# Kernel optimization log

Hardware: AMD Instinct MI355X
Metric: run time of the kernel (lower is better)

## Reference

```python
import jax, jax.numpy as jnp
import numpy as np

N = 50000        # nodes
E = 800000       # edges (avg degree 16)
NFEAT = 16       # 14 feat + 2 pos
NHID = 64
NCLASS = 1
NGRAPHS = 500
NLAYERS = 5
DT, ALPHA, GAMMA = 1.0, 1.0, 1.0


def _lin_init(k, fan_in, fan_out):
    # torch nn.Linear default: U(-1/sqrt(fan_in), 1/sqrt(fan_in))
    lim = 1.0 / np.sqrt(fan_in)
    kw, kb = jax.random.split(k)
    W = jax.random.uniform(kw, (fan_in, fan_out), minval=-lim, maxval=lim, dtype=jnp.float32)
    b = jax.random.uniform(kb, (fan_out,), minval=-lim, maxval=lim, dtype=jnp.float32)
    return W, b


def setup_inputs() -> dict:
    key = jax.random.key(0)
    ks = jax.random.split(key, 8)
    x = jax.random.normal(ks[0], (N, 14), dtype=jnp.float32)
    pos = jax.random.normal(ks[1], (N, 2), dtype=jnp.float32)
    edge_index = jax.random.randint(ks[2], (2, E), 0, N, dtype=jnp.int64)
    batch = jnp.sort(jax.random.randint(ks[3], (N,), 0, NGRAPHS, dtype=jnp.int64))
    enc_W, enc_b = _lin_init(ks[4], NFEAT, NHID)
    conv_W, conv_b = _lin_init(ks[5], NHID, NHID)
    res_W, res_b = _lin_init(ks[6], NHID, NHID)
    dec_W, dec_b = _lin_init(ks[7], NHID, NCLASS)
    return dict(x=x, pos=pos, edge_index=edge_index, batch=batch,
                enc_W=enc_W, enc_b=enc_b, conv_W=conv_W, conv_b=conv_b,
                res_W=res_W, res_b=res_b, dec_W=dec_W, dec_b=dec_b)


def _gcn_conv(h, src, dst, W, b):
    # PyG GCNConv: add self-loops, symmetric normalization, scatter-add to dst.
    loop = jnp.arange(N, dtype=src.dtype)
    src2 = jnp.concatenate([src, loop])
    dst2 = jnp.concatenate([dst, loop])
    deg = jax.ops.segment_sum(jnp.ones_like(dst2, dtype=h.dtype), dst2, num_segments=N)
    dinv = jnp.where(deg > 0, jax.lax.rsqrt(deg), 0.0)
    hW = h @ W                                   # [N, nhid]
    norm = dinv[src2] * dinv[dst2]               # [E+N]
    msg = hW[src2] * norm[:, None]               # [E+N, nhid]
    return jax.ops.segment_sum(msg, dst2, num_segments=N) + b


def reference(x, pos, edge_index, batch, enc_W, enc_b, conv_W, conv_b, res_W, res_b, dec_W, dec_b):
    src, dst = edge_index[0], edge_index[1]
    inp = jnp.concatenate([x, pos], axis=-1)     # [N, nfeat]
    Y = inp @ enc_W + enc_b
    X = Y
    # dropout p=0 -> identity (eval mode)
    for _ in range(NLAYERS):
        agg = _gcn_conv(X, src, dst, conv_W, conv_b) + (X @ res_W + res_b)
        Y = Y + DT * (jax.nn.relu(agg) - ALPHA * Y - GAMMA * X)
        X = X + DT * Y
    Xo = X @ dec_W + dec_b                       # [N, 1]
    pooled = jax.ops.segment_sum(Xo, batch, num_segments=NGRAPHS)  # [G, 1]
    return pooled.squeeze(-1)                    # [G]
```

## Files before the change

### kernel.cpp

```cpp
#include <hip/hip_runtime.h>

#define NN 50000
#define NE 800000
#define NH 64
#define NG 500
#define NPAD 50176
#define NBKT 782
#define CAP 1536
#define ZR NN
#define SH 25088

typedef __attribute__((ext_vector_type(8))) short bf16x8;
typedef __attribute__((ext_vector_type(4))) float f32x4;

__device__ __forceinline__ unsigned short f2bf(float f) {
  unsigned x = __float_as_uint(f);
  unsigned r = ((x >> 16) & 1u) + 0x7fffu;
  return (unsigned short)((x + r) >> 16);
}
__device__ __forceinline__ float bf2f(unsigned short u) {
  return __uint_as_float(((unsigned)u) << 16);
}


__global__ __launch_bounds__(256) void k_prep(const float* __restrict__ Wc, const float* __restrict__ Wr,
                                              unsigned short* __restrict__ Wf,
                                              int* __restrict__ bcur,
                                              unsigned short* __restrict__ hWbf) {
  if (blockIdx.x == 8) {
    int tt = threadIdx.x;
    for (int i = tt; i < 1024; i += 256) bcur[i] = 0;
    if (tt < 32) ((unsigned*)(hWbf + (size_t)ZR * 64))[tt] = 0u;
    return;
  }
  int t = blockIdx.x * 256 + threadIdx.x;
  int fid = t >> 6;
  int lane = t & 63;
  int ntile = fid & 3, s = (fid >> 2) & 1, part = (fid >> 3) & 1, mat = fid >> 4;
  const float* W = mat ? Wr : Wc;
  int col = ntile * 16 + (lane & 15);
  int k0 = s * 32 + (lane >> 4) * 8;
#pragma unroll
  for (int e = 0; e < 8; e++) {
    float w = W[(k0 + e) * 64 + col];
    unsigned short h = f2bf(w);
    Wf[(size_t)fid * 512 + lane * 8 + e] = part ? f2bf(w - bf2f(h)) : h;
  }
}


__global__ __launch_bounds__(256) void k_bin(const int* __restrict__ src, const int* __restrict__ dst,
                                             int* __restrict__ bcur, int* __restrict__ colp) {
  __shared__ int hist[NBKT];
  __shared__ int gbase[NBKT];
  int t = threadIdx.x;
  for (int b = t; b < NBKT; b += 256) hist[b] = 0;
  __syncthreads();
  int e0 = blockIdx.x * 8192;
#pragma unroll
  for (int i = 0; i < 32; i++) {
    int e = e0 + i * 256 + t;
    if (e < NE) atomicAdd(&hist[dst[e] >> 6], 1);
  }
  __syncthreads();
  for (int b = t; b < NBKT; b += 256) {
    int c = hist[b];
    gbase[b] = c ? atomicAdd(&bcur[b], c) : 0;
    hist[b] = 0;
  }
  __syncthreads();
#pragma unroll
  for (int i = 0; i < 32; i++) {
    int e = e0 + i * 256 + t;
    if (e < NE) {
      int s = src[e], d = dst[e];
      int b = d >> 6;
      int r = atomicAdd(&hist[b], 1);
      colp[b * CAP + gbase[b] + r] = (s << 6) | (d & 63);
    }
  }
}


template <int MODE>
__device__ __forceinline__ void gemm_tile(int lane, int n0,
                                          const float* __restrict__ Xin,
                                          const unsigned short* __restrict__ gsum,
                                          const unsigned short* __restrict__ Wf,
                                          const float* __restrict__ cb, const float* __restrict__ rb,
                                          const float* __restrict__ dinv,
                                          unsigned short* __restrict__ hWout, float* __restrict__ agg) {
  int col16 = lane & 15;
  int kb = lane >> 4;
  int nr = n0 + col16;
  int nc = nr < NN ? nr : NN - 1;
  const float* xrow = Xin + (size_t)nc * 64;
  float v0[8], v1[8];
  {
    float4 a = *(const float4*)(xrow + kb * 8);
    float4 b4 = *(const float4*)(xrow + kb * 8 + 4);
    float4 c = *(const float4*)(xrow + 32 + kb * 8);
    float4 d = *(const float4*)(xrow + 32 + kb * 8 + 4);
    v0[0] = a.x; v0[1] = a.y; v0[2] = a.z; v0[3] = a.w;
    v0[4] = b4.x; v0[5] = b4.y; v0[6] = b4.z; v0[7] = b4.w;
    v1[0] = c.x; v1[1] = c.y; v1[2] = c.z; v1[3] = c.w;
    v1[4] = d.x; v1[5] = d.y; v1[6] = d.z; v1[7] = d.w;
  }
  if (MODE) {
    float dvn = dinv[nc];
    const unsigned* grow = (const unsigned*)(gsum + (size_t)nc * 64);
    uint4 g0 = *(const uint4*)(grow + kb * 4);
    uint4 g1 = *(const uint4*)(grow + 16 + kb * 4);
    unsigned ga[4] = {g0.x, g0.y, g0.z, g0.w};
    unsigned gb[4] = {g1.x, g1.y, g1.z, g1.w};
#pragma unroll
    for (int e = 0; e < 4; e++) {
      v0[2 * e]     = fmaxf(v0[2 * e]     + dvn * bf2f((unsigned short)(ga[e] & 0xffff)), 0.f);
      v0[2 * e + 1] = fmaxf(v0[2 * e + 1] + dvn * bf2f((unsigned short)(ga[e] >> 16)), 0.f);
      v1[2 * e]     = fmaxf(v1[2 * e]     + dvn * bf2f((unsigned short)(gb[e] & 0xffff)), 0.f);
      v1[2 * e + 1] = fmaxf(v1[2 * e + 1] + dvn * bf2f((unsigned short)(gb[e] >> 16)), 0.f);
    }
  }
  bf16x8 ah0, al0, ah1, al1;
#pragma unroll
  for (int e = 0; e < 8; e++) {
    unsigned short h0 = f2bf(v0[e]);
    ah0[e] = (short)h0;
    al0[e] = (short)f2bf(v0[e] - bf2f(h0));
    unsigned short h1 = f2bf(v1[e]);
    ah1[e] = (short)h1;
    al1[e] = (short)f2bf(v1[e] - bf2f(h1));
  }

  f32x4 aC[4], aR[4];
#pragma unroll
  for (int j = 0; j < 4; j++) {
    aC[j] = (f32x4){0.f, 0.f, 0.f, 0.f};
    aR[j] = (f32x4){0.f, 0.f, 0.f, 0.f};
  }
  const bf16x8* WFv = (const bf16x8*)Wf;
#pragma unroll
  for (int j = 0; j < 4; j++) {
    bf16x8 wch0 = WFv[(j)      * 64 + lane];
    bf16x8 wch1 = WFv[(4 + j)  * 64 + lane];
    bf16x8 wcl0 = WFv[(8 + j)  * 64 + lane];
    bf16x8 wcl1 = WFv[(12 + j) * 64 + lane];
    bf16x8 wrh0 = WFv[(16 + j) * 64 + lane];
    bf16x8 wrh1 = WFv[(20 + j) * 64 + lane];
    bf16x8 wrl0 = WFv[(24 + j) * 64 + lane];
    bf16x8 wrl1 = WFv[(28 + j) * 64 + lane];
    f32x4 c = aC[j];
    c = __builtin_amdgcn_mfma_f32_16x16x32_bf16(ah0, wch0, c, 0, 0, 0);
    c = __builtin_amdgcn_mfma_f32_16x16x32_bf16(ah1, wch1, c, 0, 0, 0);
    c = __builtin_amdgcn_mfma_f32_16x16x32_bf16(al0, wch0, c, 0, 0, 0);
    c = __builtin_amdgcn_mfma_f32_16x16x32_bf16(al1, wch1, c, 0, 0, 0);
    c = __builtin_amdgcn_mfma_f32_16x16x32_bf16(ah0, wcl0, c, 0, 0, 0);
    c = __builtin_amdgcn_mfma_f32_16x16x32_bf16(ah1, wcl1, c, 0, 0, 0);
    aC[j] = c;
    f32x4 r = aR[j];
    r = __builtin_amdgcn_mfma_f32_16x16x32_bf16(ah0, wrh0, r, 0, 0, 0);
    r = __builtin_amdgcn_mfma_f32_16x16x32_bf16(ah1, wrh1, r, 0, 0, 0);
    r = __builtin_amdgcn_mfma_f32_16x16x32_bf16(al0, wrh0, r, 0, 0, 0);
    r = __builtin_amdgcn_mfma_f32_16x16x32_bf16(al1, wrh1, r, 0, 0, 0);
    r = __builtin_amdgcn_mfma_f32_16x16x32_bf16(ah0, wrl0, r, 0, 0, 0);
    r = __builtin_amdgcn_mfma_f32_16x16x32_bf16(ah1, wrl1, r, 0, 0, 0);
    aR[j] = r;
  }

  float cbv[4], rbv[4];
#pragma unroll
  for (int j = 0; j < 4; j++) {
    cbv[j] = cb[j * 16 + col16];
    rbv[j] = rb[j * 16 + col16];
  }
  int rbase = kb * 4;
#pragma unroll
  for (int r = 0; r < 4; r++) {
    int node = n0 + rbase + r;
    if (node < NN) {
      float dv = dinv[node];
      size_t o = (size_t)node * 64 + col16;
#pragma unroll
      for (int j = 0; j < 4; j++) {
        float hc = dv * aC[j][r];
        unsigned short hb = f2bf(hc);
        hWout[o + j * 16] = hb;
        agg[o + j * 16] = aR[j][r] + rbv[j] + cbv[j] + dv * hc;
      }
    }
  }
}


__global__ __launch_bounds__(256) void k_csr_enc_g0(const int* __restrict__ bcur, const int* __restrict__ colp,
                                                    int* __restrict__ cols, float* __restrict__ dinv,
                                                    int2* __restrict__ rows2, int* __restrict__ midg,
                                                    const int* __restrict__ batch, int* __restrict__ gptr,
                                                    const float* __restrict__ x, const float* __restrict__ pos,
                                                    const float* __restrict__ encW, const float* __restrict__ encb,
                                                    const unsigned short* __restrict__ Wf,
                                                    const float* __restrict__ cb, const float* __restrict__ rb,
                                                    unsigned short* __restrict__ hWout,
                                                    float* __restrict__ X0, float* __restrict__ agg) {
  __shared__ int h0c[64], h1c[64];
  __shared__ int excl[65];
  __shared__ int midS[64];
  __shared__ float Ws[16 * 64];
  __shared__ float bs[64];
  int t = threadIdx.x;
  int b = blockIdx.x;

  int tid = b * 256 + t;
  if (tid < NN) {
    int bi = batch[tid];
    int bp = (tid > 0) ? batch[tid - 1] : -1;
    for (int g = bp + 1; g <= bi; g++) gptr[g] = tid;
    if (tid == NN - 1) {
      for (int g = bi + 1; g <= NG; g++) gptr[g] = NN;
    }
  }

  for (int i = t; i < 1024; i += 256) Ws[i] = encW[i];
  if (t < 64) bs[t] = encb[t];

  int base = b * CAP;
  int cnt = bcur[b];
  if (t < 64) { h0c[t] = 0; h1c[t] = 0; }
  __syncthreads();
  for (int e = t; e < cnt; e += 256) {
    int w = colp[base + e];
    if ((w >> 6) < SH) atomicAdd(&h0c[w & 63], 1); else atomicAdd(&h1c[w & 63], 1);
  }
  __syncthreads();
  if (t == 0) {
    int run = 0;
#pragma unroll
    for (int i = 0; i < 64; i++) { excl[i] = run; run += h0c[i] + h1c[i]; }
    excl[64] = run;
  }
  __syncthreads();
  if (t < 64) {
    int n = b * 64 + t;
    rows2[n] = make_int2(base + excl[t], base + excl[t + 1]);
    int m = excl[t] + h0c[t];
    midS[t] = m;
    midg[n] = base + m;
    if (n < NN) dinv[n] = rsqrtf((float)(h0c[t] + h1c[t] + 1));
  }
  __syncthreads();
  if (t < 64) { h0c[t] = 0; h1c[t] = 0; }
  __syncthreads();
  for (int e = t; e < cnt; e += 256) {
    int w = colp[base + e];
    int d = w & 63, s = w >> 6;
    if (s < SH) {
      int r = atomicAdd(&h0c[d], 1);
      cols[base + excl[d] + r] = s;
    } else {
      int r = atomicAdd(&h1c[d], 1);
      cols[base + midS[d] + r] = s;
    }
  }

  int h = t & 63;
  int nset = t >> 6;
#pragma unroll
  for (int i = 0; i < 16; i++) {
    int n = b * 64 + nset * 16 + i;
    if (n < NN) {
      const float* xr = x + n * 14;
      float acc = bs[h];
#pragma unroll
      for (int f = 0; f < 14; f++) acc += xr[f] * Ws[f * 64 + h];
      acc += pos[n * 2 + 0] * Ws[14 * 64 + h];
      acc += pos[n * 2 + 1] * Ws[15 * 64 + h];
      X0[(size_t)n * 64 + h] = acc;
    }
  }
  __syncthreads();

  gemm_tile<0>(t & 63, b * 64 + (t >> 6) * 16, X0, (const unsigned short*)0, Wf, cb, rb, dinv, hWout, agg);
}


__global__ __launch_bounds__(256) void k_gemm(const float* __restrict__ Xin,
                                              const unsigned short* __restrict__ gsum,
                                              const unsigned short* __restrict__ Wf,
                                              const float* __restrict__ cb, const float* __restrict__ rb,
                                              const float* __restrict__ dinv,
                                              unsigned short* __restrict__ hWout, float* __restrict__ agg) {
  gemm_tile<1>(threadIdx.x & 63, blockIdx.x * 64 + (threadIdx.x >> 6) * 16,
               Xin, gsum, Wf, cb, rb, dinv, hWout, agg);
}


__device__ __forceinline__ void gather_seg(int st, int en, int lane, int h2, int p,
                                           const int* __restrict__ cols, const unsigned* __restrict__ hW32,
                                           float& a0, float& a1) {
  int deg = en - st;
  a0 = 0.f; a1 = 0.f;
  for (int base2 = 0; base2 < deg; base2 += 64) {
    int cnt = deg - base2;
    if (cnt > 64) cnt = 64;
    int li = lane < cnt ? lane : cnt - 1;
    int colv = cols[st + base2 + li];
    for (int j = 0; j < cnt; j += 16) {
      int sx[8];
#pragma unroll
      for (int k2 = 0; k2 < 8; k2++) {
        int e = j + 2 * k2 + p;
        int s = __shfl(colv, e, 64);
        sx[k2] = e < cnt ? s : ZR;
      }
      unsigned ux[8];
#pragma unroll
      for (int k2 = 0; k2 < 8; k2++) ux[k2] = hW32[(unsigned)sx[k2] * 32u + (unsigned)h2];
#pragma unroll
      for (int k2 = 0; k2 < 8; k2++) {
        a0 += __uint_as_float(ux[k2] << 16);
        a1 += __uint_as_float(ux[k2] & 0xffff0000u);
      }
    }
  }
  a0 += __shfl_down(a0, 32, 64);
  a1 += __shfl_down(a1, 32, 64);
}


__global__ __launch_bounds__(256, 8) void k_gather_p0(const int2* __restrict__ rows2, const int* __restrict__ midg,
                                                      const int* __restrict__ cols,
                                                      const unsigned short* __restrict__ hWin,
                                                      float* __restrict__ gpart) {
  int lane = threadIdx.x & 63;
  int h2 = lane & 31;
  int p = lane >> 5;
  int n = __builtin_amdgcn_readfirstlane(blockIdx.x * 4 + (threadIdx.x >> 6));
  float a0, a1;
  gather_seg(rows2[n].x, midg[n], lane, h2, p, cols, (const unsigned*)hWin, a0, a1);
  if (lane < 32) {
    float* gp = gpart + ((size_t)n * 32 + h2) * 2;
    __builtin_nontemporal_store(a0, gp);
    __builtin_nontemporal_store(a1, gp + 1);
  }
}


__global__ __launch_bounds__(256, 8) void k_gather_p1(const int2* __restrict__ rows2, const int* __restrict__ midg,
                                                      const int* __restrict__ cols,
                                                      const unsigned short* __restrict__ hWin,
                                                      const float* __restrict__ gpart,
                                                      unsigned short* __restrict__ gsum) {
  int lane = threadIdx.x & 63;
  int h2 = lane & 31;
  int p = lane >> 5;
  int n = __builtin_amdgcn_readfirstlane(blockIdx.x * 4 + (threadIdx.x >> 6));
  float a0, a1;
  gather_seg(midg[n], rows2[n].y, lane, h2, p, cols, (const unsigned*)hWin, a0, a1);
  if (lane < 32) {
    const float* gp = gpart + ((size_t)n * 32 + h2) * 2;
    a0 += __builtin_nontemporal_load(gp);
    a1 += __builtin_nontemporal_load(gp + 1);
    ((unsigned*)gsum)[(unsigned)n * 32u + (unsigned)h2] = (unsigned)f2bf(a0) | ((unsigned)f2bf(a1) << 16);
  }
}


__global__ __launch_bounds__(256, 8) void k_gather_f1(const int2* __restrict__ rows2, const int* __restrict__ midg,
                                                      const int* __restrict__ cols,
                                                      const unsigned short* __restrict__ hWin,
                                                      const float* __restrict__ gpart,
                                                      const float* __restrict__ aggIn, const float* __restrict__ dinv,
                                                      const float* __restrict__ decW, float* __restrict__ Xo) {
  int lane = threadIdx.x & 63;
  int h2 = lane & 31;
  int p = lane >> 5;
  int n = __builtin_amdgcn_readfirstlane(blockIdx.x * 4 + (threadIdx.x >> 6));
  float a0, a1;
  gather_seg(midg[n], rows2[n].y, lane, h2, p, cols, (const unsigned*)hWin, a0, a1);
  const float* gp = gpart + ((size_t)n * 32 + h2) * 2;
  a0 += __builtin_nontemporal_load(gp);
  a1 += __builtin_nontemporal_load(gp + 1);
  float dv = dinv[n];
  float2 ag = *(const float2*)(aggIn + (size_t)n * 64 + h2 * 2);
  float v = fmaxf(ag.x + dv * a0, 0.f) * decW[h2 * 2] + fmaxf(ag.y + dv * a1, 0.f) * decW[h2 * 2 + 1];
  v = (lane < 32) ? v : 0.f;
#pragma unroll
  for (int off = 32; off > 0; off >>= 1) v += __shfl_down(v, off, 64);
  if (lane == 0) Xo[n] = v;
}


__global__ __launch_bounds__(256) void k_pool(const float* __restrict__ Xo, const int* __restrict__ gptr,
                                              const float* __restrict__ decb, float* __restrict__ out) {
  __shared__ float part[4];
  int g = blockIdx.x;
  int t = threadIdx.x;
  int st = gptr[g], en = gptr[g + 1];
  float v = 0.f;
  for (int i = st + t; i < en; i += 256) v += Xo[i];
#pragma unroll
  for (int off = 32; off > 0; off >>= 1) v += __shfl_down(v, off, 64);
  if ((t & 63) == 0) part[t >> 6] = v;
  __syncthreads();
  if (t == 0) out[g] = part[0] + part[1] + part[2] + part[3] + (float)(en - st) * decb[0];
}


extern "C" void kernel_launch(void* const* d_in, const int* in_sizes, int n_in,
                              void* d_out, int out_size, void* d_ws, size_t ws_size,
                              hipStream_t stream) {
  (void)in_sizes; (void)n_in; (void)out_size; (void)ws_size;
  const float* x     = (const float*)d_in[0];
  const float* pos   = (const float*)d_in[1];
  const int*   ei    = (const int*)d_in[2];
  const int*   batch = (const int*)d_in[3];
  const float* encW  = (const float*)d_in[4];
  const float* encb  = (const float*)d_in[5];
  const float* convW = (const float*)d_in[6];
  const float* convb = (const float*)d_in[7];
  const float* resW  = (const float*)d_in[8];
  const float* resb  = (const float*)d_in[9];
  const float* decW  = (const float*)d_in[10];
  const float* decb  = (const float*)d_in[11];
  float* out = (float*)d_out;

  const int* src = ei;
  const int* dst = ei + NE;

  float*          ws    = (float*)d_ws;
  float*          dinv  = ws;
  int2*           rows2 = (int2*)(ws + NPAD);
  int*            midg  = (int*)(ws + 3 * NPAD);
  int*            bcur  = (int*)(ws + 4 * NPAD);
  int*            gptr  = bcur + 1024;
  float*          Xo    = (float*)(gptr + 512);
  int*            colp  = (int*)(Xo + NPAD);
  int*            cols  = colp + NBKT * CAP;
  unsigned short* hWbf  = (unsigned short*)(cols + NBKT * CAP);
  unsigned short* gsum  = hWbf + (size_t)NPAD * 64;
  float*          gpart = (float*)(gsum + (size_t)NPAD * 64);
  float*          bufA  = gpart + (size_t)NPAD * 64;
  float*          bufB  = bufA + NN * NH;
  unsigned short* Wf    = (unsigned short*)(bufB + NN * NH);

  k_prep<<<9, 256, 0, stream>>>(convW, resW, Wf, bcur, hWbf);
  k_bin<<<(NE + 8191) / 8192, 256, 0, stream>>>(src, dst, bcur, colp);
  k_csr_enc_g0<<<NBKT, 256, 0, stream>>>(bcur, colp, cols, dinv, rows2, midg, batch, gptr,
                                         x, pos, encW, encb, Wf, convb, resb,
                                         hWbf, bufA, bufB);
  float* aggIn = bufB;
  float* aggOut = bufA;
  for (int l = 0; l < 4; l++) {
    k_gather_p0<<<NN / 4, 256, 0, stream>>>(rows2, midg, cols, hWbf, gpart);
    k_gather_p1<<<NN / 4, 256, 0, stream>>>(rows2, midg, cols, hWbf, gpart, gsum);
    k_gemm<<<NBKT, 256, 0, stream>>>(aggIn, gsum, Wf, convb, resb, dinv, hWbf, aggOut);
    float* tmp = aggIn; aggIn = aggOut; aggOut = tmp;
  }
  k_gather_p0<<<NN / 4, 256, 0, stream>>>(rows2, midg, cols, hWbf, gpart);
  k_gather_f1<<<NN / 4, 256, 0, stream>>>(rows2, midg, cols, hWbf, gpart, aggIn, dinv, decW, Xo);
  k_pool<<<NG, 256, 0, stream>>>(Xo, gptr, decb, out);
}
```

Measured before the change: 336.9 us.

## Fuse two-phase gather into persistent kernel with grid barrier and LDS partials

Replaces the separate gather_p0/p1 (and final f1) launches with one persistent kernel where each wave handles 13 nodes. The first-phase partial sums are kept in shared memory, and a software grid-wide barrier orders the two phases. This removes a launch per layer and the global gpart write/read. In exchange it relies on all 1024 blocks being co-resident, adds barrier spin cost and lowers occupancy. It also makes the column index loads nontemporal.

```diff
diff --git a/kernel.cpp b/kernel.cpp
--- a/kernel.cpp
+++ b/kernel.cpp
@@ -9,6 +9,8 @@
 #define CAP 1536
 #define ZR NN
 #define SH 25088
+#define NBLK 1024
+#define NPW 13
 
 typedef __attribute__((ext_vector_type(8))) short bf16x8;
 typedef __attribute__((ext_vector_type(4))) float f32x4;
@@ -303,7 +305,7 @@
     int cnt = deg - base2;
     if (cnt > 64) cnt = 64;
     int li = lane < cnt ? lane : cnt - 1;
-    int colv = cols[st + base2 + li];
+    int colv = __builtin_nontemporal_load(cols + st + base2 + li);
     for (int j = 0; j < cnt; j += 16) {
       int sx[8];
 #pragma unroll
@@ -327,66 +329,68 @@
 }
 
 
-__global__ __launch_bounds__(256, 8) void k_gather_p0(const int2* __restrict__ rows2, const int* __restrict__ midg,
-                                                      const int* __restrict__ cols,
-                                                      const unsigned short* __restrict__ hWin,
-                                                      float* __restrict__ gpart) {
-  int lane = threadIdx.x & 63;
-  int h2 = lane & 31;
-  int p = lane >> 5;
-  int n = __builtin_amdgcn_readfirstlane(blockIdx.x * 4 + (threadIdx.x >> 6));
-  float a0, a1;
-  gather_seg(rows2[n].x, midg[n], lane, h2, p, cols, (const unsigned*)hWin, a0, a1);
-  if (lane < 32) {
-    float* gp = gpart + ((size_t)n * 32 + h2) * 2;
-    __builtin_nontemporal_store(a0, gp);
-    __builtin_nontemporal_store(a1, gp + 1);
-  }
-}
-
-
-__global__ __launch_bounds__(256, 8) void k_gather_p1(const int2* __restrict__ rows2, const int* __restrict__ midg,
-                                                      const int* __restrict__ cols,
-                                                      const unsigned short* __restrict__ hWin,
-                                                      const float* __restrict__ gpart,
-                                                      unsigned short* __restrict__ gsum) {
-  int lane = threadIdx.x & 63;
-  int h2 = lane & 31;
-  int p = lane >> 5;
-  int n = __builtin_amdgcn_readfirstlane(blockIdx.x * 4 + (threadIdx.x >> 6));
-  float a0, a1;
-  gather_seg(midg[n], rows2[n].y, lane, h2, p, cols, (const unsigned*)hWin, a0, a1);
-  if (lane < 32) {
-    const float* gp = gpart + ((size_t)n * 32 + h2) * 2;
-    a0 += __builtin_nontemporal_load(gp);
-    a1 += __builtin_nontemporal_load(gp + 1);
-    ((unsigned*)gsum)[(unsigned)n * 32u + (unsigned)h2] = (unsigned)f2bf(a0) | ((unsigned)f2bf(a1) << 16);
-  }
-}
-
-
-__global__ __launch_bounds__(256, 8) void k_gather_f1(const int2* __restrict__ rows2, const int* __restrict__ midg,
-                                                      const int* __restrict__ cols,
-                                                      const unsigned short* __restrict__ hWin,
-                                                      const float* __restrict__ gpart,
-                                                      const float* __restrict__ aggIn, const float* __restrict__ dinv,
-                                                      const float* __restrict__ decW, float* __restrict__ Xo) {
-  int lane = threadIdx.x & 63;
-  int h2 = lane & 31;
-  int p = lane >> 5;
-  int n = __builtin_amdgcn_readfirstlane(blockIdx.x * 4 + (threadIdx.x >> 6));
-  float a0, a1;
-  gather_seg(midg[n], rows2[n].y, lane, h2, p, cols, (const unsigned*)hWin, a0, a1);
-  const float* gp = gpart + ((size_t)n * 32 + h2) * 2;
-  a0 += __builtin_nontemporal_load(gp);
-  a1 += __builtin_nontemporal_load(gp + 1);
-  float dv = dinv[n];
-  float2 ag = *(const float2*)(aggIn + (size_t)n * 64 + h2 * 2);
-  float v = fmaxf(ag.x + dv * a0, 0.f) * decW[h2 * 2] + fmaxf(ag.y + dv * a1, 0.f) * decW[h2 * 2 + 1];
-  v = (lane < 32) ? v : 0.f;
-#pragma unroll
-  for (int off = 32; off > 0; off >>= 1) v += __shfl_down(v, off, 64);
-  if (lane == 0) Xo[n] = v;
+__global__ __launch_bounds__(256, 4) void k_gather2(const int2* __restrict__ rows2, const int* __restrict__ midg,
+                                                    const int* __restrict__ cols,
+                                                    const unsigned short* __restrict__ hWin,
+                                                    unsigned short* __restrict__ gsum,
+                                                    const float* __restrict__ aggIn, const float* __restrict__ dinv,
+                                                    const float* __restrict__ decW, float* __restrict__ Xo,
+                                                    int* __restrict__ bar_cnt, volatile int* bar_gen, int last) {
+  __shared__ float pA[2][4][NPW][32];
+  int t = threadIdx.x;
+  int lane = t & 63, h2 = lane & 31, p = lane >> 5, wv = t >> 6;
+  int nb = (blockIdx.x * 4 + wv) * NPW;
+  const unsigned* hW32 = (const unsigned*)hWin;
+
+#pragma unroll 1
+  for (int i = 0; i < NPW; i++) {
+    int n = nb + i;
+    if (n < NN) {
+      float a0, a1;
+      gather_seg(rows2[n].x, midg[n], lane, h2, p, cols, hW32, a0, a1);
+      if (lane < 32) { pA[0][wv][i][h2] = a0; pA[1][wv][i][h2] = a1; }
+    }
+  }
+
+  __syncthreads();
+  if (t == 0) {
+    int g = *bar_gen;
+    int v = atomicAdd(bar_cnt, 1);
+    if (v == NBLK - 1) {
+      *bar_cnt = 0;
+      __threadfence();
+      atomicAdd((int*)bar_gen, 1);
+    } else {
+      while (*bar_gen == g) __builtin_amdgcn_s_sleep(16);
+    }
+  }
+  __syncthreads();
+
+#pragma unroll 1
+  for (int i = 0; i < NPW; i++) {
+    int n = nb + i;
+    if (n < NN) {
+      float a0, a1;
+      gather_seg(midg[n], rows2[n].y, lane, h2, p, cols, hW32, a0, a1);
+      a0 += pA[0][wv][i][h2];
+      a1 += pA[1][wv][i][h2];
+      if (!last) {
+        if (lane < 32)
+          __builtin_nontemporal_store((unsigned)f2bf(a0) | ((unsigned)f2bf(a1) << 16),
+                                      (unsigned*)gsum + (size_t)n * 32 + h2);
+      } else {
+        float dv = dinv[n];
+        float2 ag;
+        ag.x = __builtin_nontemporal_load(aggIn + (size_t)n * 64 + h2 * 2);
+        ag.y = __builtin_nontemporal_load(aggIn + (size_t)n * 64 + h2 * 2 + 1);
+        float v = fmaxf(ag.x + dv * a0, 0.f) * decW[h2 * 2] + fmaxf(ag.y + dv * a1, 0.f) * decW[h2 * 2 + 1];
+        v = (lane < 32) ? v : 0.f;
+#pragma unroll
+        for (int off = 32; off > 0; off >>= 1) v += __shfl_down(v, off, 64);
+        if (lane == 0) Xo[n] = v;
+      }
+    }
+  }
 }
 
 
@@ -438,10 +442,12 @@
   int*            cols  = colp + NBKT * CAP;
   unsigned short* hWbf  = (unsigned short*)(cols + NBKT * CAP);
   unsigned short* gsum  = hWbf + (size_t)NPAD * 64;
-  float*          gpart = (float*)(gsum + (size_t)NPAD * 64);
-  float*          bufA  = gpart + (size_t)NPAD * 64;
+  float*          bufA  = (float*)(gsum + (size_t)NPAD * 64);
   float*          bufB  = bufA + NN * NH;
   unsigned short* Wf    = (unsigned short*)(bufB + NN * NH);
+
+  int* bar_cnt = bcur + 800;
+  volatile int* bar_gen = (volatile int*)(bcur + 801);
 
   k_prep<<<9, 256, 0, stream>>>(convW, resW, Wf, bcur, hWbf);
   k_bin<<<(NE + 8191) / 8192, 256, 0, stream>>>(src, dst, bcur, colp);
@@ -451,12 +457,12 @@
   float* aggIn = bufB;
   float* aggOut = bufA;
   for (int l = 0; l < 4; l++) {
-    k_gather_p0<<<NN / 4, 256, 0, stream>>>(rows2, midg, cols, hWbf, gpart);
-    k_gather_p1<<<NN / 4, 256, 0, stream>>>(rows2, midg, cols, hWbf, gpart, gsum);
+    k_gather2<<<NBLK, 256, 0, stream>>>(rows2, midg, cols, hWbf, gsum,
+                                        (const float*)0, dinv, decW, (float*)0, bar_cnt, bar_gen, 0);
     k_gemm<<<NBKT, 256, 0, stream>>>(aggIn, gsum, Wf, convb, resb, dinv, hWbf, aggOut);
     float* tmp = aggIn; aggIn = aggOut; aggOut = tmp;
   }
-  k_gather_p0<<<NN / 4, 256, 0, stream>>>(rows2, midg, cols, hWbf, gpart);
-  k_gather_f1<<<NN / 4, 256, 0, stream>>>(rows2, midg, cols, hWbf, gpart, aggIn, dinv, decW, Xo);
+  k_gather2<<<NBLK, 256, 0, stream>>>(rows2, midg, cols, hWbf, gsum,
+                                      aggIn, dinv, decW, Xo, bar_cnt, bar_gen, 1);
   k_pool<<<NG, 256, 0, stream>>>(Xo, gptr, decb, out);
 }
```

New measurement: 693.2 us. 106% more time.
